# Kernel optimization log

Hardware: AMD Instinct MI355X
Metric: run time of the kernel (lower is better)

## Reference

```python
import jax, jax.numpy as jnp
import numpy as np
import math

TAU = 1.0          # args.gumbel_tau, used as GMM variance scale in assign()
RD = 64            # args.reduce_dimension
NE = 8             # args.dynamic_nexperts
COMMIT = 0.1       # args.commitment_scale
T, B, C, O = 2048, 8, 512, 512


def setup_inputs() -> dict:
    key = jax.random.key(0)
    ks = jax.random.split(key, 9)
    a = math.sqrt(6.0) / (C + O)  # init for pw_w per dynamic_init_method==1
    return {
        "x": jax.random.normal(ks[0], (T, B, C), jnp.float32),
        "key_feat": jax.random.normal(ks[1], (T, B, C), jnp.float32),  # ignored by forward
        "map_w": jax.random.normal(ks[2], (RD, C), jnp.float32) * math.sqrt(2.0 / (C + RD)),
        "map_b": jnp.zeros((RD,), jnp.float32),
        "centroids": jax.random.normal(ks[3], (NE, RD), jnp.float32) * 0.02,
        "prior": jnp.ones((1, NE), jnp.float32) / NE,
        "pw_w": jax.random.uniform(ks[4], (NE, O * C), jnp.float32, -a, a),
        "bias_w": jax.random.normal(ks[5], (O, C), jnp.float32) * 0.02,
        "bias_b": jnp.zeros((O,), jnp.float32),
    }


def reference(x, key_feat, map_w, map_b, centroids, prior, pw_w, bias_w, bias_b):
    # x: [T, B, C] time-major. key_feat is ignored, matching the original forward.
    Tq, Bq, Cq = x.shape
    N = Tq * Bq
    xf = x.reshape(N, Cq)
    # GMM key projection: [N, RD]
    k = xf @ map_w.T + map_b
    # squared euclid distance to centroids: [N, NE]
    d2 = (jnp.sum(k * k, axis=1, keepdims=True)
          + jnp.sum(centroids * centroids, axis=1)[None, :]
          - 2.0 * (k @ centroids.T))
    # soft GMM responsibilities (training path, no gumbel sampling)
    logresp = (-0.5 * TAU * d2
               - (RD / 2.0) * math.log(2.0 * math.pi * TAU)
               + jnp.log(prior))                                  # [N, NE]
    denom = jax.scipy.special.logsumexp(logresp, axis=-1, keepdims=True)
    resp = jnp.exp(logresp - denom)                               # [N, NE]
    loss = COMMIT * (-jnp.sum(denom))
    # Expert mixture. Original: w = (resp @ pw_w).reshape(T,B,O,C); y = w @ x.
    # Same math, fused order: apply each expert to x, then mix with resp.
    W = pw_w.reshape(NE, O, Cq)
    z = jnp.einsum('ni,eoi->neo', xf, W)        # [N, NE, O] per-expert outputs
    y = jnp.einsum('ne,neo->no', resp, z)       # [N, O]
    y = y.reshape(Tq, Bq, O)
    # dynamic bias: Linear(key_dim -> O) applied to x0
    y = y + x @ bias_w.T + bias_b
    return y, loss
```

## Files before the change

### kernel.cpp

```cpp
#include <hip/hip_runtime.h>
#include <hip/hip_bf16.h>

#define NROWS 16384
#define CC 512
#define OO 512
#define RDIM 64
#define NE 8
#define NEXP 9
#define COMMIT_SCALE 0.1f
#define LOG2PI_TERM 58.81206612509905f

typedef __attribute__((ext_vector_type(8))) short short8;
typedef __attribute__((ext_vector_type(4))) float f32x4;

__device__ __forceinline__ unsigned short f2bf(float f) {
  unsigned int u = __float_as_uint(f);
  u += 0x7fffu + ((u >> 16) & 1u);
  return (unsigned short)(u >> 16);
}
__device__ __forceinline__ unsigned int pkt(float a, float b) {
  return (__float_as_uint(b) & 0xffff0000u) | (__float_as_uint(a) >> 16);
}

__device__ __forceinline__ void gl_lds16(const unsigned short* g, unsigned short* l) {
  __builtin_amdgcn_global_load_lds(
      (const __attribute__((address_space(1))) void*)g,
      (__attribute__((address_space(3))) void*)l, 16, 0, 0);
}

#define P4 524288u
#define B4 65536u
#define NCV ((P4 + B4) / 256u)
#define TB 128u

__global__ __launch_bounds__(256) void k_prep(
    const float* __restrict__ pw, const float* __restrict__ bw,
    const float* __restrict__ mw,
    unsigned short* __restrict__ wb, float* __restrict__ wT4)
{
  unsigned int b = blockIdx.x;
  if (b >= NCV) {
    unsigned int i = (b - NCV) * 256 + threadIdx.x;
    unsigned int j = i >> 9, c = i & 511u;
    wT4[((c >> 2) << 8) + (j << 2) + (c & 3u)] = mw[i];
    return;
  }
  unsigned int i = b * 256 + threadIdx.x;
  const float* src = (i < P4) ? (pw + (size_t)i * 4)
                              : (bw + (size_t)(i - P4) * 4);
  unsigned short* dst = wb + (size_t)i * 4;
  float4 v = *(const float4*)src;
  ushort4 o;
  o.x = f2bf(v.x); o.y = f2bf(v.y); o.z = f2bf(v.z); o.w = f2bf(v.w);
  *(ushort4*)dst = o;
}

__global__ __launch_bounds__(256) void k_assign(
    const float* __restrict__ x,
    const float* __restrict__ wT4,
    const float* __restrict__ map_b,
    const float* __restrict__ cent,
    const float* __restrict__ prior,
    float* __restrict__ resp_out,
    float* __restrict__ loss_acc)
{
  __shared__ float lsum[4];
  const int tid  = threadIdx.x;
  const int wid  = tid >> 6;
  const int lane = tid & 63;
  const int row0 = blockIdx.x * 16 + wid * 4;

  const float* xr0 = x + (size_t)row0 * CC;
  float acc[4] = {0.f, 0.f, 0.f, 0.f};
  #pragma unroll 4
  for (int c0 = 0; c0 < CC; c0 += 4) {
    float4 wv = *(const float4*)&wT4[(c0 << 6) + (lane << 2)];
    #pragma unroll
    for (int r = 0; r < 4; ++r) {
      float4 xv = *(const float4*)(xr0 + r * CC + c0);
      acc[r] += xv.x * wv.x + xv.y * wv.y + xv.z * wv.z + xv.w * wv.w;
    }
  }
  const float mb = map_b[lane];
  float kk[4] = {acc[0] + mb, acc[1] + mb, acc[2] + mb, acc[3] + mb};

  float ce[8], c2[8], lp[8];
  #pragma unroll
  for (int e = 0; e < 8; ++e) {
    ce[e] = cent[e * RDIM + lane];
    float v = ce[e] * ce[e];
    #pragma unroll
    for (int off = 32; off; off >>= 1) v += __shfl_xor(v, off, 64);
    c2[e] = v;
    lp[e] = __logf(prior[e]);
  }

  float dsum = 0.f;
  #pragma unroll
  for (int r = 0; r < 4; ++r) {
    float k = kk[r];
    float v[9];
    v[0] = k * k;
    #pragma unroll
    for (int e = 0; e < 8; ++e) v[e + 1] = k * ce[e];
    #pragma unroll
    for (int off = 32; off; off >>= 1) {
      #pragma unroll
      for (int q = 0; q < 9; ++q) v[q] += __shfl_xor(v[q], off, 64);
    }
    float lr[8], mx = -3.4e38f;
    #pragma unroll
    for (int e = 0; e < 8; ++e) {
      float d2 = v[0] + c2[e] - 2.f * v[e + 1];
      lr[e] = -0.5f * d2 - LOG2PI_TERM + lp[e];
      mx = fmaxf(mx, lr[e]);
    }
    float s = 0.f;
    #pragma unroll
    for (int e = 0; e < 8; ++e) s += __expf(lr[e] - mx);
    float denom = mx + __logf(s);
    dsum += denom;
    float myv = 0.f;
    #pragma unroll
    for (int e = 0; e < 8; ++e) {
      float re = __expf(lr[e] - denom);
      myv = (lane == e) ? re : myv;
    }
    if (lane < 8) resp_out[(size_t)(row0 + r) * NE + lane] = myv;
  }
  if (lane == 0) lsum[wid] = dsum;
  __syncthreads();
  if (tid == 0) {
    float t = lsum[0] + lsum[1] + lsum[2] + lsum[3];
    atomicAdd(loss_acc, -COMMIT_SCALE * t);
  }
}

__global__ __launch_bounds__(256, 2) void k_moe(
    const float* __restrict__ x,
    const unsigned short* __restrict__ wb,
    const float* __restrict__ bb,
    const float* __restrict__ resp,
    const float* __restrict__ loss_acc,
    float* __restrict__ out)
{
  __shared__ __align__(16) unsigned short aT[128 * 64];
  __shared__ __align__(16) unsigned short bT[2][128 * 64];
  __shared__ float sc[NE * 128];

  const int tid = threadIdx.x;
  const int m0 = blockIdx.x * 128;
  const int o0 = blockIdx.y * 128;
  const int lane = tid & 63;
  const int wid = tid >> 6;
  const int fr = lane & 15;
  const int fq = lane >> 4;

  for (int idx = tid; idx < 128 * NE; idx += 256) {
    int r = idx >> 3, e = idx & 7;
    sc[e * 128 + r] = resp[(size_t)(m0 + r) * NE + e];
  }

  const int rl = lane >> 3;
  const int ch = lane & 7;
  const unsigned short* wb_t =
      wb + (size_t)(o0 + wid * 32 + rl) * CC + (ch ^ rl) * 8;

  const int ar = tid >> 1;
  const int ah = tid & 1;
  const float* xa = x + (size_t)(m0 + ar) * CC + ah * 32;

  const int s7 = fr & 7;
  const int ac0 = (fq ^ s7) * 8;

  const f32x4 zero4 = {0.f, 0.f, 0.f, 0.f};
  f32x4 ySum[8][2];
  #pragma unroll
  for (int i = 0; i < 8; ++i) {
    ySum[i][0] = zero4; ySum[i][1] = zero4;
  }

  {
    const float4* xp = (const float4*)xa;
    #pragma unroll
    for (int q = 0; q < 4; ++q) {
      float4 f0 = xp[2 * q], f1 = xp[2 * q + 1];
      uint4 w;
      w.x = pkt(f0.x, f0.y); w.y = pkt(f0.z, f0.w);
      w.z = pkt(f1.x, f1.y); w.w = pkt(f1.z, f1.w);
      *(uint4*)&aT[ar * 64 + (((ah * 4 + q) ^ (ar & 7)) << 3)] = w;
    }
    #pragma unroll
    for (int q = 0; q < 4; ++q)
      gl_lds16(wb_t + q * 4096, &bT[0][wid * 2048 + q * 512]);
  }

  short8 af[16];
  float4 xf[8];
  int cur = 0;

  #pragma unroll 1
  for (int kk = 0; kk < 8; ++kk) {
    #pragma unroll 1
    for (int e = 0; e < NEXP; ++e) {
      __syncthreads();

      if (e < 8 || kk < 7) {
        const int ne = (e < 8) ? e + 1 : 0;
        const int nk = (e < 8) ? kk : kk + 1;
        const unsigned short* bn = wb_t + ((size_t)ne << 18) + nk * 64;
        #pragma unroll
        for (int q = 0; q < 4; ++q)
          gl_lds16(bn + q * 4096, &bT[cur ^ 1][wid * 2048 + q * 512]);
      }

      if (e == 0) {
        #pragma unroll
        for (int i = 0; i < 8; ++i) {
          const int rb = (i * 16 + fr) * 64;
          af[2 * i]     = *(const short8*)&aT[rb + ac0];
          af[2 * i + 1] = *(const short8*)&aT[rb + (ac0 ^ 32)];
        }
        if (kk < 7) {
          const float4* xp = (const float4*)(xa + (kk + 1) * 64);
          #pragma unroll
          for (int q = 0; q < 8; ++q) xf[q] = xp[q];
        }
      } else if (e == 1 && kk < 7) {
        #pragma unroll
        for (int q = 0; q < 4; ++q) {
          uint4 w;
          w.x = pkt(xf[2 * q].x,     xf[2 * q].y);
          w.y = pkt(xf[2 * q].z,     xf[2 * q].w);
          w.z = pkt(xf[2 * q + 1].x, xf[2 * q + 1].y);
          w.w = pkt(xf[2 * q + 1].z, xf[2 * q + 1].w);
          *(uint4*)&aT[ar * 64 + (((ah * 4 + q) ^ (ar & 7)) << 3)] = w;
        }
      }

      short8 bfv[4];
      const unsigned short* bc = &bT[cur][0];
      #pragma unroll
      for (int j = 0; j < 2; ++j) {
        const int rb = (wid * 32 + j * 16 + fr) * 64;
        bfv[2 * j]     = *(const short8*)&bc[rb + ac0];
        bfv[2 * j + 1] = *(const short8*)&bc[rb + (ac0 ^ 32)];
      }

      if (e < 8) {
        #pragma unroll
        for (int i = 0; i < 8; ++i) {
          const f32x4 s = *(const f32x4*)&sc[e * 128 + i * 16 + fq * 4];
          #pragma unroll
          for (int j = 0; j < 2; ++j) {
            f32x4 t = __builtin_amdgcn_mfma_f32_16x16x32_bf16(
                af[2 * i], bfv[2 * j], zero4, 0, 0, 0);
            t = __builtin_amdgcn_mfma_f32_16x16x32_bf16(
                af[2 * i + 1], bfv[2 * j + 1], t, 0, 0, 0);
            ySum[i][j] += s * t;
          }
        }
      } else {
        #pragma unroll
        for (int i = 0; i < 8; ++i) {
          #pragma unroll
          for (int j = 0; j < 2; ++j) {
            ySum[i][j] = __builtin_amdgcn_mfma_f32_16x16x32_bf16(
                af[2 * i], bfv[2 * j], ySum[i][j], 0, 0, 0);
            ySum[i][j] = __builtin_amdgcn_mfma_f32_16x16x32_bf16(
                af[2 * i + 1], bfv[2 * j + 1], ySum[i][j], 0, 0, 0);
          }
        }
      }
      cur ^= 1;
    }
  }

  #pragma unroll
  for (int j = 0; j < 2; ++j) {
    const int o = o0 + wid * 32 + j * 16 + fr;
    const float bias = bb[o];
    #pragma unroll
    for (int i = 0; i < 8; ++i) {
      #pragma unroll
      for (int r = 0; r < 4; ++r) {
        int m = m0 + i * 16 + fq * 4 + r;
        out[(size_t)m * OO + o] = ySum[i][j][r] + bias;
      }
    }
  }

  if (blockIdx.x == 0 && blockIdx.y == 0 && tid == 0)
    out[(size_t)NROWS * OO] = loss_acc[0];
}

extern "C" void kernel_launch(void* const* d_in, const int* in_sizes, int n_in,
                              void* d_out, int out_size, void* d_ws, size_t ws_size,
                              hipStream_t stream) {
  const float* x     = (const float*)d_in[0];
  const float* map_w = (const float*)d_in[2];
  const float* map_b = (const float*)d_in[3];
  const float* cent  = (const float*)d_in[4];
  const float* prior = (const float*)d_in[5];
  const float* pw    = (const float*)d_in[6];
  const float* bw    = (const float*)d_in[7];
  const float* bb    = (const float*)d_in[8];
  float* out = (float*)d_out;

  char* wsp = (char*)d_ws;
  float* resp = (float*)wsp;
  float* loss = (float*)(wsp + 524288);
  unsigned short* wb = (unsigned short*)(wsp + 524304);
  float* wT4 = (float*)(wsp + 524304 + 4718592);

  hipMemsetAsync(loss, 0, sizeof(float), stream);
  k_prep<<<dim3(NCV + TB), dim3(256), 0, stream>>>(pw, bw, map_w, wb, wT4);
  k_assign<<<dim3(NROWS / 16), dim3(256), 0, stream>>>(x, wT4, map_b, cent, prior, resp, loss);
  dim3 grid(NROWS / 128, OO / 128);
  k_moe<<<grid, dim3(256), 0, stream>>>(x, wb, bb, resp, loss, out);
}
```

Measured before the change: 311.1 us.

## Triple-buffer expert weight tiles with explicit vmcnt waits and raised MFMA priority

Replaces the double-buffered B tile with a three-stage ring, so weight loads are issued two steps ahead. The per-step __syncthreads is replaced by hand-counted s_waitcnt vmcnt values plus a raw s_barrier at the end of each step. The x prefetch for the next k-chunk is moved earlier so it stays outside the waitcnt accounting. s_setprio is raised around the MFMA block to favour compute issue. This adds 16KB of LDS, which may reduce occupancy below two blocks per CU. The hand-tuned vmcnt counts are fragile if the compiler reorders or splits loads.

```diff
diff --git a/kernel.cpp b/kernel.cpp
--- a/kernel.cpp
+++ b/kernel.cpp
@@ -145,7 +145,7 @@
     float* __restrict__ out)
 {
   __shared__ __align__(16) unsigned short aT[128 * 64];
-  __shared__ __align__(16) unsigned short bT[2][128 * 64];
+  __shared__ __align__(16) unsigned short bT[3][128 * 64];
   __shared__ float sc[NE * 128];
 
   const int tid = threadIdx.x;
@@ -190,28 +190,58 @@
       w.z = pkt(f1.x, f1.y); w.w = pkt(f1.z, f1.w);
       *(uint4*)&aT[ar * 64 + (((ah * 4 + q) ^ (ar & 7)) << 3)] = w;
     }
-    #pragma unroll
-    for (int q = 0; q < 4; ++q)
-      gl_lds16(wb_t + q * 4096, &bT[0][wid * 2048 + q * 512]);
-  }
+  }
+  __syncthreads();
+
+  float4 xf[8];
+  {
+    const float4* xp = (const float4*)(xa + 64);
+    #pragma unroll
+    for (int q = 0; q < 8; ++q) xf[q] = xp[q];
+  }
+  asm volatile("" ::: "memory");
+  #pragma unroll
+  for (int q = 0; q < 4; ++q)
+    gl_lds16(wb_t + q * 4096, &bT[0][wid * 2048 + q * 512]);
+  #pragma unroll
+  for (int q = 0; q < 4; ++q)
+    gl_lds16(wb_t + ((size_t)1 << 18) + q * 4096, &bT[1][wid * 2048 + q * 512]);
 
   short8 af[16];
-  float4 xf[8];
   int cur = 0;
 
   #pragma unroll 1
   for (int kk = 0; kk < 8; ++kk) {
     #pragma unroll 1
     for (int e = 0; e < NEXP; ++e) {
-      __syncthreads();
-
-      if (e < 8 || kk < 7) {
-        const int ne = (e < 8) ? e + 1 : 0;
-        const int nk = (e < 8) ? kk : kk + 1;
-        const unsigned short* bn = wb_t + ((size_t)ne << 18) + nk * 64;
-        #pragma unroll
-        for (int q = 0; q < 4; ++q)
-          gl_lds16(bn + q * 4096, &bT[cur ^ 1][wid * 2048 + q * 512]);
+      if (e == 8 && kk <= 5) {
+        const float4* xp = (const float4*)(xa + (kk + 2) * 64);
+        #pragma unroll
+        for (int q = 0; q < 8; ++q) xf[q] = xp[q];
+        asm volatile("" ::: "memory");
+      }
+
+      {
+        int ne = e + 2, nk = kk;
+        if (ne >= NEXP) { ne -= NEXP; ++nk; }
+        if (nk <= 7) {
+          const int wnx = (cur >= 1) ? cur - 1 : 2;
+          const unsigned short* bn =
+              wb_t + ((size_t)ne << 18) + (size_t)nk * 64;
+          #pragma unroll
+          for (int q = 0; q < 4; ++q)
+            gl_lds16(bn + q * 4096, &bT[wnx][wid * 2048 + q * 512]);
+        }
+      }
+
+      if ((e == 8 && kk <= 5) || (e == 0 && kk >= 1 && kk <= 6)) {
+        asm volatile("s_waitcnt vmcnt(16)" ::: "memory");
+      } else if (kk == 7 && e == 7) {
+        asm volatile("s_waitcnt vmcnt(4)" ::: "memory");
+      } else if (kk == 7 && e == 8) {
+        asm volatile("s_waitcnt vmcnt(0)" ::: "memory");
+      } else {
+        asm volatile("s_waitcnt vmcnt(8)" ::: "memory");
       }
 
       if (e == 0) {
@@ -220,11 +250,6 @@
           const int rb = (i * 16 + fr) * 64;
           af[2 * i]     = *(const short8*)&aT[rb + ac0];
           af[2 * i + 1] = *(const short8*)&aT[rb + (ac0 ^ 32)];
-        }
-        if (kk < 7) {
-          const float4* xp = (const float4*)(xa + (kk + 1) * 64);
-          #pragma unroll
-          for (int q = 0; q < 8; ++q) xf[q] = xp[q];
         }
       } else if (e == 1 && kk < 7) {
         #pragma unroll
@@ -247,6 +272,7 @@
         bfv[2 * j + 1] = *(const short8*)&bc[rb + (ac0 ^ 32)];
       }
 
+      __builtin_amdgcn_s_setprio(1);
       if (e < 8) {
         #pragma unroll
         for (int i = 0; i < 8; ++i) {
@@ -272,7 +298,10 @@
           }
         }
       }
-      cur ^= 1;
+      __builtin_amdgcn_s_setprio(0);
+
+      __builtin_amdgcn_s_barrier();
+      cur = (cur == 2) ? 0 : cur + 1;
     }
   }
 
```

Result: slower. 332.6 us (+6.9%).

## Load MoE GEMM operands directly into registers, dropping LDS staging and barriers

Applied to the files above, without the earlier changes.

The MoE GEMM kernel now reads x and the bf16 expert weights straight from global memory into MFMA operand registers, with a register double buffer for the weight fragments. This removes the LDS tiles and the per-step __syncthreads. The block tile changes from 128x128 to 256 rows by 64 outputs, and all four waves share the same 64 output columns across different rows. The aim is to cut LDS traffic and barrier stalls. In exchange, every wave issues redundant global/L2 loads for the same weight fragments, and register pressure rises under the launch bound of 2 blocks.

```diff
diff --git a/kernel.cpp b/kernel.cpp
--- a/kernel.cpp
+++ b/kernel.cpp
@@ -20,12 +20,6 @@
 }
 __device__ __forceinline__ unsigned int pkt(float a, float b) {
   return (__float_as_uint(b) & 0xffff0000u) | (__float_as_uint(a) >> 16);
-}
-
-__device__ __forceinline__ void gl_lds16(const unsigned short* g, unsigned short* l) {
-  __builtin_amdgcn_global_load_lds(
-      (const __attribute__((address_space(1))) void*)g,
-      (__attribute__((address_space(3))) void*)l, 16, 0, 0);
 }
 
 #define P4 524288u
@@ -144,147 +138,158 @@
     const float* __restrict__ loss_acc,
     float* __restrict__ out)
 {
-  __shared__ __align__(16) unsigned short aT[128 * 64];
-  __shared__ __align__(16) unsigned short bT[2][128 * 64];
-  __shared__ float sc[NE * 128];
+  __shared__ float sc[NE * 256];
 
   const int tid = threadIdx.x;
-  const int m0 = blockIdx.x * 128;
-  const int o0 = blockIdx.y * 128;
+  const int m0 = blockIdx.x * 256;
+  const int o0 = blockIdx.y * 64;
   const int lane = tid & 63;
   const int wid = tid >> 6;
   const int fr = lane & 15;
   const int fq = lane >> 4;
 
-  for (int idx = tid; idx < 128 * NE; idx += 256) {
+  for (int idx = tid; idx < 256 * NE; idx += 256) {
     int r = idx >> 3, e = idx & 7;
-    sc[e * 128 + r] = resp[(size_t)(m0 + r) * NE + e];
-  }
-
-  const int rl = lane >> 3;
-  const int ch = lane & 7;
-  const unsigned short* wb_t =
-      wb + (size_t)(o0 + wid * 32 + rl) * CC + (ch ^ rl) * 8;
-
-  const int ar = tid >> 1;
-  const int ah = tid & 1;
-  const float* xa = x + (size_t)(m0 + ar) * CC + ah * 32;
-
-  const int s7 = fr & 7;
-  const int ac0 = (fq ^ s7) * 8;
+    sc[e * 256 + r] = resp[(size_t)(m0 + r) * NE + e];
+  }
+  __syncthreads();
+
+  const float* xk = x + (size_t)(m0 + wid * 64 + fr) * CC + fq * 8;
+  const unsigned short* bk = wb + (size_t)(o0 + fr) * CC + fq * 8;
 
   const f32x4 zero4 = {0.f, 0.f, 0.f, 0.f};
-  f32x4 ySum[8][2];
-  #pragma unroll
-  for (int i = 0; i < 8; ++i) {
-    ySum[i][0] = zero4; ySum[i][1] = zero4;
-  }
-
-  {
-    const float4* xp = (const float4*)xa;
-    #pragma unroll
-    for (int q = 0; q < 4; ++q) {
-      float4 f0 = xp[2 * q], f1 = xp[2 * q + 1];
-      uint4 w;
-      w.x = pkt(f0.x, f0.y); w.y = pkt(f0.z, f0.w);
-      w.z = pkt(f1.x, f1.y); w.w = pkt(f1.z, f1.w);
-      *(uint4*)&aT[ar * 64 + (((ah * 4 + q) ^ (ar & 7)) << 3)] = w;
-    }
-    #pragma unroll
-    for (int q = 0; q < 4; ++q)
-      gl_lds16(wb_t + q * 4096, &bT[0][wid * 2048 + q * 512]);
-  }
-
-  short8 af[16];
-  float4 xf[8];
-  int cur = 0;
+  f32x4 ySum[4][4];
+  #pragma unroll
+  for (int i = 0; i < 4; ++i)
+    #pragma unroll
+    for (int j = 0; j < 4; ++j) ySum[i][j] = zero4;
+
+  short8 af[8];
+  short8 bA[8], bB[8];
+
+  #pragma unroll
+  for (int ip = 0; ip < 2; ++ip) {
+    float4 t0[2][2], t1[2][2];
+    #pragma unroll
+    for (int iw = 0; iw < 2; ++iw) {
+      const int i = ip * 2 + iw;
+      #pragma unroll
+      for (int h = 0; h < 2; ++h) {
+        const float4* pp = (const float4*)(xk + i * 8192 + h * 32);
+        t0[iw][h] = pp[0]; t1[iw][h] = pp[1];
+      }
+    }
+    #pragma unroll
+    for (int iw = 0; iw < 2; ++iw) {
+      const int i = ip * 2 + iw;
+      #pragma unroll
+      for (int h = 0; h < 2; ++h) {
+        uint4 w;
+        w.x = pkt(t0[iw][h].x, t0[iw][h].y);
+        w.y = pkt(t0[iw][h].z, t0[iw][h].w);
+        w.z = pkt(t1[iw][h].x, t1[iw][h].y);
+        w.w = pkt(t1[iw][h].z, t1[iw][h].w);
+        af[2 * i + h] = *(short8*)&w;
+      }
+    }
+  }
+  #pragma unroll
+  for (int j = 0; j < 4; ++j)
+    #pragma unroll
+    for (int h = 0; h < 2; ++h)
+      bA[2 * j + h] = *(const short8*)(bk + j * 8192 + h * 32);
 
   #pragma unroll 1
-  for (int kk = 0; kk < 8; ++kk) {
-    #pragma unroll 1
-    for (int e = 0; e < NEXP; ++e) {
-      __syncthreads();
-
-      if (e < 8 || kk < 7) {
-        const int ne = (e < 8) ? e + 1 : 0;
-        const int nk = (e < 8) ? kk : kk + 1;
-        const unsigned short* bn = wb_t + ((size_t)ne << 18) + nk * 64;
-        #pragma unroll
-        for (int q = 0; q < 4; ++q)
-          gl_lds16(bn + q * 4096, &bT[cur ^ 1][wid * 2048 + q * 512]);
-      }
-
-      if (e == 0) {
-        #pragma unroll
-        for (int i = 0; i < 8; ++i) {
-          const int rb = (i * 16 + fr) * 64;
-          af[2 * i]     = *(const short8*)&aT[rb + ac0];
-          af[2 * i + 1] = *(const short8*)&aT[rb + (ac0 ^ 32)];
+  for (int kk2 = 0; kk2 < 4; ++kk2) {
+    #pragma unroll
+    for (int p = 0; p < 18; ++p) {
+      const int e = p % 9;
+      short8* bc = (p & 1) ? bB : bA;
+      short8* bn = (p & 1) ? bA : bB;
+
+      if (e < 8) {
+        #pragma unroll
+        for (int j = 0; j < 4; ++j)
+          #pragma unroll
+          for (int h = 0; h < 2; ++h)
+            bn[2 * j + h] = *(const short8*)(
+                bk + (size_t)(e + 1) * 262144 + j * 8192 + h * 32);
+      } else if (p == 8 || kk2 < 3) {
+        #pragma unroll
+        for (int j = 0; j < 4; ++j)
+          #pragma unroll
+          for (int h = 0; h < 2; ++h)
+            bn[2 * j + h] = *(const short8*)(bk + 64 + j * 8192 + h * 32);
+      }
+
+      if (e < 8) {
+        f32x4 si[4];
+        #pragma unroll
+        for (int i = 0; i < 4; ++i)
+          si[i] = *(const f32x4*)&sc[e * 256 + wid * 64 + i * 16 + fq * 4];
+        #pragma unroll
+        for (int i = 0; i < 4; ++i)
+          #pragma unroll
+          for (int j = 0; j < 4; ++j) {
+            f32x4 t = __builtin_amdgcn_mfma_f32_16x16x32_bf16(
+                af[2 * i], bc[2 * j], zero4, 0, 0, 0);
+            t = __builtin_amdgcn_mfma_f32_16x16x32_bf16(
+                af[2 * i + 1], bc[2 * j + 1], t, 0, 0, 0);
+            ySum[i][j] += si[i] * t;
+          }
+      } else {
+        #pragma unroll
+        for (int i = 0; i < 4; ++i)
+          #pragma unroll
+          for (int j = 0; j < 4; ++j) {
+            ySum[i][j] = __builtin_amdgcn_mfma_f32_16x16x32_bf16(
+                af[2 * i], bc[2 * j], ySum[i][j], 0, 0, 0);
+            ySum[i][j] = __builtin_amdgcn_mfma_f32_16x16x32_bf16(
+                af[2 * i + 1], bc[2 * j + 1], ySum[i][j], 0, 0, 0);
+          }
+        if (p == 8 || kk2 < 3) {
+          #pragma unroll
+          for (int ip = 0; ip < 2; ++ip) {
+            float4 t0[2][2], t1[2][2];
+            #pragma unroll
+            for (int iw = 0; iw < 2; ++iw) {
+              const int i = ip * 2 + iw;
+              #pragma unroll
+              for (int h = 0; h < 2; ++h) {
+                const float4* pp = (const float4*)(xk + 64 + i * 8192 + h * 32);
+                t0[iw][h] = pp[0]; t1[iw][h] = pp[1];
+              }
+            }
+            #pragma unroll
+            for (int iw = 0; iw < 2; ++iw) {
+              const int i = ip * 2 + iw;
+              #pragma unroll
+              for (int h = 0; h < 2; ++h) {
+                uint4 w;
+                w.x = pkt(t0[iw][h].x, t0[iw][h].y);
+                w.y = pkt(t0[iw][h].z, t0[iw][h].w);
+                w.z = pkt(t1[iw][h].x, t1[iw][h].y);
+                w.w = pkt(t1[iw][h].z, t1[iw][h].w);
+                af[2 * i + h] = *(short8*)&w;
+              }
+            }
+          }
+          xk += 64;
         }
-        if (kk < 7) {
-          const float4* xp = (const float4*)(xa + (kk + 1) * 64);
-          #pragma unroll
-          for (int q = 0; q < 8; ++q) xf[q] = xp[q];
-        }
-      } else if (e == 1 && kk < 7) {
-        #pragma unroll
-        for (int q = 0; q < 4; ++q) {
-          uint4 w;
-          w.x = pkt(xf[2 * q].x,     xf[2 * q].y);
-          w.y = pkt(xf[2 * q].z,     xf[2 * q].w);
-          w.z = pkt(xf[2 * q + 1].x, xf[2 * q + 1].y);
-          w.w = pkt(xf[2 * q + 1].z, xf[2 * q + 1].w);
-          *(uint4*)&aT[ar * 64 + (((ah * 4 + q) ^ (ar & 7)) << 3)] = w;
-        }
-      }
-
-      short8 bfv[4];
-      const unsigned short* bc = &bT[cur][0];
-      #pragma unroll
-      for (int j = 0; j < 2; ++j) {
-        const int rb = (wid * 32 + j * 16 + fr) * 64;
-        bfv[2 * j]     = *(const short8*)&bc[rb + ac0];
-        bfv[2 * j + 1] = *(const short8*)&bc[rb + (ac0 ^ 32)];
-      }
-
-      if (e < 8) {
-        #pragma unroll
-        for (int i = 0; i < 8; ++i) {
-          const f32x4 s = *(const f32x4*)&sc[e * 128 + i * 16 + fq * 4];
-          #pragma unroll
-          for (int j = 0; j < 2; ++j) {
-            f32x4 t = __builtin_amdgcn_mfma_f32_16x16x32_bf16(
-                af[2 * i], bfv[2 * j], zero4, 0, 0, 0);
-            t = __builtin_amdgcn_mfma_f32_16x16x32_bf16(
-                af[2 * i + 1], bfv[2 * j + 1], t, 0, 0, 0);
-            ySum[i][j] += s * t;
-          }
-        }
-      } else {
-        #pragma unroll
-        for (int i = 0; i < 8; ++i) {
-          #pragma unroll
-          for (int j = 0; j < 2; ++j) {
-            ySum[i][j] = __builtin_amdgcn_mfma_f32_16x16x32_bf16(
-                af[2 * i], bfv[2 * j], ySum[i][j], 0, 0, 0);
-            ySum[i][j] = __builtin_amdgcn_mfma_f32_16x16x32_bf16(
-                af[2 * i + 1], bfv[2 * j + 1], ySum[i][j], 0, 0, 0);
-          }
-        }
-      }
-      cur ^= 1;
-    }
-  }
-
-  #pragma unroll
-  for (int j = 0; j < 2; ++j) {
-    const int o = o0 + wid * 32 + j * 16 + fr;
+        bk += 64;
+      }
+    }
+  }
+
+  #pragma unroll
+  for (int j = 0; j < 4; ++j) {
+    const int o = o0 + j * 16 + fr;
     const float bias = bb[o];
     #pragma unroll
-    for (int i = 0; i < 8; ++i) {
+    for (int i = 0; i < 4; ++i) {
       #pragma unroll
       for (int r = 0; r < 4; ++r) {
-        int m = m0 + i * 16 + fq * 4 + r;
+        int m = m0 + wid * 64 + i * 16 + fq * 4 + r;
         out[(size_t)m * OO + o] = ySum[i][j][r] + bias;
       }
     }
@@ -316,6 +321,6 @@
   hipMemsetAsync(loss, 0, sizeof(float), stream);
   k_prep<<<dim3(NCV + TB), dim3(256), 0, stream>>>(pw, bw, map_w, wb, wT4);
   k_assign<<<dim3(NROWS / 16), dim3(256), 0, stream>>>(x, wT4, map_b, cent, prior, resp, loss);
-  dim3 grid(NROWS / 128, OO / 128);
+  dim3 grid(NROWS / 256, OO / 64);
   k_moe<<<grid, dim3(256), 0, stream>>>(x, wb, bb, resp, loss, out);
 }
```

Measured after the change: 1.161 ms. +273.1%, slower.
